# Performance work log

Measured on AMD Instinct MI355X. Metric: run time of the kernel, lower is better.

Reference implementation:

```python
import jax, jax.numpy as jnp
import numpy as np
import math

B, T, C, F = 8, 2048, 1024, 4096
N_LAYER, LAYER_ID = 12, 1


def _init_params(key):
    ks = jax.random.split(key, 16)
    s = 0.02
    ratio_0_to_1 = LAYER_ID / (N_LAYER - 1)
    ratio_1_to_almost0 = 1.0 - LAYER_ID / N_LAYER
    h = np.arange(C, dtype=np.float32)
    decay = -5.0 + 8.0 * (h / (C - 1)) ** (0.7 + 1.3 * ratio_0_to_1)
    zigzag = np.array([((i + 1) % 3 - 1) for i in range(C)], dtype=np.float32) * 0.5
    first = np.ones(C, dtype=np.float32) * math.log(0.3) + zigzag
    xi = (np.arange(C, dtype=np.float32) / C)
    p = {
        'ln1_w': jnp.ones(C), 'ln1_b': jnp.zeros(C),
        'ln2_w': jnp.ones(C), 'ln2_b': jnp.zeros(C),
        'att_time_decay': jnp.asarray(decay),
        'att_time_first': jnp.asarray(first),
        'att_mix_k': jnp.asarray(xi ** ratio_1_to_almost0),
        'att_mix_v': jnp.asarray(xi ** ratio_1_to_almost0 + 0.3 * ratio_0_to_1),
        'att_mix_r': jnp.asarray(xi ** (0.5 * ratio_1_to_almost0)),
        'att_Wk': jax.random.normal(ks[0], (C, C)) * s,
        'att_Wv': jax.random.normal(ks[1], (C, C)) * s,
        'att_Wr': jax.random.normal(ks[2], (C, C)) * s,
        'att_Wo': jax.random.normal(ks[3], (C, C)) * s,
        'ffn_mix_k': jnp.asarray(xi ** ratio_1_to_almost0),
        'ffn_mix_r': jnp.asarray(xi ** ratio_1_to_almost0),
        'ffn_Wk': jax.random.normal(ks[4], (F, C)) * s,
        'ffn_Wr': jax.random.normal(ks[5], (C, C)) * s,
        'ffn_Wv': jax.random.normal(ks[6], (C, F)) * s,
        'short_W': jax.random.normal(ks[7], (C, C)) * s,
    }
    return p


def setup_inputs() -> dict:
    key = jax.random.key(0)
    k1, k2 = jax.random.split(key)
    inp = {'x': jax.random.normal(k1, (B, T, C), dtype=jnp.float32)}
    inp.update(_init_params(k2))
    return inp


def _layernorm(x, w, b, eps=1e-5):
    mu = jnp.mean(x, axis=-1, keepdims=True)
    var = jnp.var(x, axis=-1, keepdims=True)
    return (x - mu) * jax.lax.rsqrt(var + eps) * w + b


def _time_shift(x):
    # ZeroPad2d((0,0,1,-1)): prepend zero row along T, drop last
    return jnp.pad(x, ((0, 0), (1, 0), (0, 0)))[:, :-1]


def _wkv(time_decay, time_first, k, v):
    # numerically-stable WKV recurrence, matching the CUDA kernel math
    w = -jnp.exp(time_decay)  # [C]
    u = time_first            # [C]
    kt = jnp.swapaxes(k, 0, 1)  # [T,B,C]
    vt = jnp.swapaxes(v, 0, 1)
    a0 = jnp.zeros(k.shape[::2] if False else (k.shape[0], k.shape[2]), k.dtype)
    b0 = jnp.zeros_like(a0)
    p0 = jnp.full_like(a0, -1e30)

    def step(carry, kv):
        a, b, p = carry
        k_t, v_t = kv
        ww = u + k_t
        q = jnp.maximum(p, ww)
        e1 = jnp.exp(p - q)
        e2 = jnp.exp(ww - q)
        y = (e1 * a + e2 * v_t) / (e1 * b + e2)
        ww2 = p + w
        q2 = jnp.maximum(ww2, k_t)
        f1 = jnp.exp(ww2 - q2)
        f2 = jnp.exp(k_t - q2)
        return (f1 * a + f2 * v_t, f1 * b + f2, q2), y

    _, ys = jax.lax.scan(step, (a0, b0, p0), (kt, vt))
    return jnp.swapaxes(ys, 0, 1)  # [B,T,C]


def _lin(x, W):
    return jnp.einsum('btc,oc->bto', x, W)


def reference(x, ln1_w, ln1_b, ln2_w, ln2_b,
              att_time_decay, att_time_first, att_mix_k, att_mix_v, att_mix_r,
              att_Wk, att_Wv, att_Wr, att_Wo,
              ffn_mix_k, ffn_mix_r, ffn_Wk, ffn_Wr, ffn_Wv, short_W):
    # --- TimeMix on ln1(x) ---
    h = _layernorm(x, ln1_w, ln1_b)
    hh = _time_shift(h)
    xk = h * att_mix_k + hh * (1 - att_mix_k)
    xv = h * att_mix_v + hh * (1 - att_mix_v)
    xr = h * att_mix_r + hh * (1 - att_mix_r)
    k = _lin(xk, att_Wk)
    v = _lin(xv, att_Wv)
    sr = jax.nn.sigmoid(_lin(xr, att_Wr))
    rwkv = sr * _wkv(att_time_decay, att_time_first, k, v)
    att_out = _lin(rwkv, att_Wo)
    # shortcut linear replaces identity residual (L3TC Block)
    x = _lin(x, short_W) + att_out
    # --- ChannelMix on ln2(x) ---
    g = _layernorm(x, ln2_w, ln2_b)
    gg = _time_shift(g)
    gk = g * ffn_mix_k + gg * (1 - ffn_mix_k)
    gr = g * ffn_mix_r + gg * (1 - ffn_mix_r)
    kk = jnp.square(jax.nn.relu(_lin(gk, ffn_Wk)))
    kv = _lin(kk, ffn_Wv)
    rkv = jax.nn.sigmoid(_lin(gr, ffn_Wr)) * kv
    return x + rkv
```

## Files before the change

### kernel.cpp

```cpp
#include <hip/hip_runtime.h>

#define BB 8
#define TT 2048
#define CC 1024
#define FF 4096
#define MM (BB*TT)

typedef unsigned short u16;
typedef __bf16 bf16x8 __attribute__((ext_vector_type(8)));
typedef float f32x4 __attribute__((ext_vector_type(4)));

__device__ __forceinline__ u16 f2bf(float f) {
  unsigned int u = __float_as_uint(f);
  u += 0x7fffu + ((u >> 16) & 1u);
  return (u16)(u >> 16);
}
__device__ __forceinline__ float bf2f(u16 h) {
  unsigned int u = ((unsigned int)h) << 16;
  return __uint_as_float(u);
}
__device__ __forceinline__ float sigm(float x) { return 1.f / (1.f + __expf(-x)); }

__device__ __forceinline__ void async16(const void* g, void* l) {
  __builtin_amdgcn_global_load_lds(
      (const __attribute__((address_space(1))) unsigned int*)g,
      (__attribute__((address_space(3))) unsigned int*)l, 16, 0, 0);
}

#define GROUP_M 16

#define DSRD(d, a, o) \
  asm volatile("ds_read_b128 %0, %1 offset:%c2" : "=v"(d) : "v"(a), "i"(o))

#define MFMA16(A_, B_, C_) \
  (C_) = __builtin_amdgcn_mfma_f32_16x16x32_bf16( \
      __builtin_bit_cast(bf16x8, (A_)), __builtin_bit_cast(bf16x8, (B_)), (C_), 0, 0, 0)

#define SCHED0  __builtin_amdgcn_sched_barrier(0)
#define BARRIER __builtin_amdgcn_s_barrier()
#define LGKM(n) asm volatile("s_waitcnt lgkmcnt(" #n ")")

#define READ_A4(bank, BETA, MH, KH) do { \
  DSRD(bank[0], aAddr##KH, (BETA)*32768 + ((MH)*4+0)*2048); \
  DSRD(bank[1], aAddr##KH, (BETA)*32768 + ((MH)*4+1)*2048); \
  DSRD(bank[2], aAddr##KH, (BETA)*32768 + ((MH)*4+2)*2048); \
  DSRD(bank[3], aAddr##KH, (BETA)*32768 + ((MH)*4+3)*2048); \
} while (0)

#define READ_B2(bank, BETA, NP, KH) do { \
  DSRD(bank[0], bAddr##KH, (BETA)*32768 + (NP)*16384 + 0*2048); \
  DSRD(bank[1], bAddr##KH, (BETA)*32768 + (NP)*16384 + 1*2048); \
} while (0)

#define MFMA8(ABANK, BBANK, AO, NO) do { \
  _Pragma("unroll") \
  for (int mi = 0; mi < 4; ++mi) \
    _Pragma("unroll") \
    for (int ni = 0; ni < 2; ++ni) \
      MFMA16(ABANK[mi], BBANK[ni], acc[(AO)+mi][(NO)+ni]); \
} while (0)

#define EXEC8(ABANK, BBANK, AO, NO) do { \
  __builtin_amdgcn_s_setprio(1); \
  MFMA8(ABANK, BBANK, AO, NO); \
  __builtin_amdgcn_s_setprio(0); SCHED0; } while (0)

#define TILE(BETA, T2A, ST, RD) do { \
   READ_A4(aB, BETA, 1, 0); \
  LGKM(6); SCHED0; EXEC8(aA, bP, 0, 0); \
   READ_B2(bR, BETA, 0, 1); \
  LGKM(6); SCHED0; EXEC8(aA, bQ, 0, 2); \
   READ_A4(aA, BETA, 0, 1); \
  LGKM(6); SCHED0; EXEC8(aB, bQ, 4, 2); \
  BARRIER; SCHED0; \
   \
  READ_B2(bS, BETA, 1, 1); \
  if (ST) { stB(BETA, 0, T2A); stB(BETA, 1, T2A); \
            stA(BETA, 0, T2A); stA(BETA, 2, T2A); } \
  LGKM(6); SCHED0; EXEC8(aB, bP, 4, 0); \
   READ_A4(aB, BETA, 1, 1); \
  LGKM(6); SCHED0; EXEC8(aA, bR, 0, 0); \
  if (ST) asm volatile("s_waitcnt vmcnt(4)"); \
  else    asm volatile("s_waitcnt vmcnt(0)"); \
  BARRIER; SCHED0; \
   \
  if (RD) READ_B2(bP, (BETA)^1, 0, 0); \
  if (ST) { stB(BETA, 2, T2A); stB(BETA, 3, T2A); \
            stA(BETA, 1, T2A); stA(BETA, 3, T2A); } \
  if (RD) LGKM(6); else LGKM(4); \
  SCHED0; EXEC8(aA, bS, 0, 2); \
   if (RD) { READ_A4(aA, (BETA)^1, 0, 0); LGKM(6); } else LGKM(0); \
  SCHED0; EXEC8(aB, bS, 4, 2); \
   if (RD) { READ_B2(bQ, (BETA)^1, 1, 0); LGKM(8); } else LGKM(0); \
  SCHED0; EXEC8(aB, bR, 4, 0); \
} while (0)

template<int MODE>
__global__ __launch_bounds__(512, 2) void gemm_bt(
    const u16* __restrict__ A, const u16* __restrict__ W,
    float* __restrict__ Cf, u16* __restrict__ Cb,
    const u16* __restrict__ R, int N, int K)
{
  __shared__ __align__(16) u16 ldsA[2][256 * 64];
  __shared__ __align__(16) u16 ldsB[2][256 * 64];

  const int tid  = threadIdx.x;
  const int wave = tid >> 6;
  const int lane = tid & 63;
  const int wmi  = wave >> 2;
  const int wni  = wave & 3;
  const int lm   = lane & 15;
  const int lq   = lane >> 4;

  const int bid  = blockIdx.x + blockIdx.y * gridDim.x;
  const int gsz  = GROUP_M * gridDim.y;
  const int gid  = bid / gsz;
  const int rem  = bid - gid * gsz;
  const int bm   = (gid * GROUP_M + (rem % GROUP_M)) * 256;
  const int bn   = (rem / GROUP_M) * 256;

  const int NT = K >> 6;

  const int ls     = lane >> 3;
  const int schunk = (lane & 7) ^ ls;
  const int rowA   = wave * 8 + ls;
  const int rowB   = (wave >> 2) * 64 + (wave & 3) * 8 + ls;
  const u16* gA = A + (size_t)(bm + rowA) * K + schunk * 8;
  const u16* gB = W + (size_t)(bn + rowB) * K + schunk * 8;
  const size_t rowK = (size_t)64 * K;

  auto stA = [&](int buf, int q, int t2) {
    async16(gA + (size_t)t2 * 64 + (size_t)q * rowK,
            &ldsA[buf][(q * 64 + wave * 8) * 64]);
  };
  auto stB = [&](int buf, int q, int t2) {
    const int qrow = (q == 0) ? 0 : (q == 1) ? 128 : (q == 2) ? 32 : 160;
    async16(gB + (size_t)t2 * 64 + (size_t)qrow * K,
            &ldsB[buf][(q * 64 + wave * 8) * 64]);
  };

  const unsigned lAbase =
      (unsigned)(size_t)(const __attribute__((address_space(3))) u16*)&ldsA[0][0];
  const unsigned lBbase =
      (unsigned)(size_t)(const __attribute__((address_space(3))) u16*)&ldsB[0][0];
  const unsigned aAddr0 = lAbase + (unsigned)((wmi * 128 + lm) * 128 + (((lq    ) ^ (lm & 7)) * 16));
  const unsigned aAddr1 = lAbase + (unsigned)((wmi * 128 + lm) * 128 + (((lq + 4) ^ (lm & 7)) * 16));
  const unsigned bAddr0 = lBbase + (unsigned)((wni * 32 + lm) * 128 + (((lq    ) ^ (lm & 7)) * 16));
  const unsigned bAddr1 = lBbase + (unsigned)((wni * 32 + lm) * 128 + (((lq + 4) ^ (lm & 7)) * 16));

  f32x4 acc[8][4] = {};
  f32x4 aA[4], aB[4], bP[2], bQ[2], bR[2], bS[2];

  stA(0, 0, 0); stA(0, 1, 0); stA(0, 2, 0); stA(0, 3, 0);
  stB(0, 0, 0); stB(0, 1, 0); stB(0, 2, 0); stB(0, 3, 0);
  stA(1, 0, 1); stA(1, 1, 1); stA(1, 2, 1); stA(1, 3, 1);
  stB(1, 0, 1); stB(1, 1, 1); stB(1, 2, 1); stB(1, 3, 1);
  asm volatile("s_waitcnt vmcnt(0)");
  BARRIER;
  READ_A4(aA, 0, 0, 0);
  READ_B2(bP, 0, 0, 0);
  READ_B2(bQ, 0, 1, 0);
  LGKM(0); SCHED0;

  for (int t = 0; t + 3 < NT; t += 2) {
    TILE(0, t + 2, 1, 1);
    TILE(1, t + 3, 1, 1);
  }

  TILE(0, 0, 0, 1);
  TILE(1, 0, 0, 0);

  const int row0 = bm + wmi * 128 + lq * 4;
  const int col0 = bn + wni * 64 + lm;
#pragma unroll
  for (int mi = 0; mi < 8; ++mi)
#pragma unroll
    for (int ni = 0; ni < 4; ++ni) {
      size_t base = (size_t)(row0 + mi * 16) * N + (col0 + ni * 16);
#pragma unroll
      for (int r2 = 0; r2 < 4; ++r2) {
        size_t idx = base + (size_t)r2 * N;
        float v = acc[mi][ni][r2];
        if (MODE == 0) Cf[idx] = v;
        if (MODE == 2) { float rl = v > 0.f ? v : 0.f; Cb[idx] = f2bf(rl * rl); }
        if (MODE == 3) Cb[idx] = f2bf(v);
        if (MODE == 4) Cf[idx] += sigm(bf2f(R[idx])) * v;
      }
    }
}

__global__ __launch_bounds__(256) void prep_mix(
    const float* __restrict__ x,
    const float* __restrict__ lnw, const float* __restrict__ lnb,
    const float* __restrict__ mk, const float* __restrict__ mv, const float* __restrict__ mr,
    u16* __restrict__ ok, u16* __restrict__ ov, u16* __restrict__ orr,
    u16* __restrict__ oxb)
{
  const int m = blockIdx.x;
  const int t = m & (TT - 1);
  const int tid = threadIdx.x;
  const int wave = tid >> 6, lane = tid & 63;
  const bool hasp = (t != 0);

  const float4 xc4 = ((const float4*)(x + (size_t)m * CC))[tid];
  float4 xp4 = make_float4(0.f, 0.f, 0.f, 0.f);
  if (hasp) xp4 = ((const float4*)(x + (size_t)(m - 1) * CC))[tid];

  float s0 = xc4.x + xc4.y + xc4.z + xc4.w;
  float s1 = xc4.x*xc4.x + xc4.y*xc4.y + xc4.z*xc4.z + xc4.w*xc4.w;
  float s2 = xp4.x + xp4.y + xp4.z + xp4.w;
  float s3 = xp4.x*xp4.x + xp4.y*xp4.y + xp4.z*xp4.z + xp4.w*xp4.w;
#pragma unroll
  for (int off2 = 32; off2 > 0; off2 >>= 1) {
    s0 += __shfl_xor(s0, off2);
    s1 += __shfl_xor(s1, off2);
    s2 += __shfl_xor(s2, off2);
    s3 += __shfl_xor(s3, off2);
  }
  __shared__ float red[4][4];
  if (lane == 0) { red[0][wave] = s0; red[1][wave] = s1; red[2][wave] = s2; red[3][wave] = s3; }
  __syncthreads();
  const float S0 = red[0][0] + red[0][1] + red[0][2] + red[0][3];
  const float S1 = red[1][0] + red[1][1] + red[1][2] + red[1][3];
  const float S2 = red[2][0] + red[2][1] + red[2][2] + red[2][3];
  const float S3 = red[3][0] + red[3][1] + red[3][2] + red[3][3];
  const float inv = 1.f / (float)CC;
  const float muc = S0 * inv, varc = S1 * inv - muc * muc, rsc = rsqrtf(varc + 1e-5f);
  const float mup = S2 * inv, varp = S3 * inv - mup * mup, rsp = rsqrtf(varp + 1e-5f);

  const float xc[4] = {xc4.x, xc4.y, xc4.z, xc4.w};
  const float xp[4] = {xp4.x, xp4.y, xp4.z, xp4.w};
  const float4 lw4 = ((const float4*)lnw)[tid];
  const float4 lb4 = ((const float4*)lnb)[tid];
  const float lw[4] = {lw4.x, lw4.y, lw4.z, lw4.w};
  const float lb[4] = {lb4.x, lb4.y, lb4.z, lb4.w};
  const float4 mk4 = ((const float4*)mk)[tid];
  const float mka[4] = {mk4.x, mk4.y, mk4.z, mk4.w};
  const float4 mr4 = ((const float4*)mr)[tid];
  const float mra[4] = {mr4.x, mr4.y, mr4.z, mr4.w};
  float mva[4] = {0.f, 0.f, 0.f, 0.f};
  if (ov) {
    const float4 mv4 = ((const float4*)mv)[tid];
    mva[0] = mv4.x; mva[1] = mv4.y; mva[2] = mv4.z; mva[3] = mv4.w;
  }

  ushort4 wk2, wv2, wr2, wb2;
  u16* pk = (u16*)&wk2; u16* pv = (u16*)&wv2; u16* pr = (u16*)&wr2; u16* pb = (u16*)&wb2;
#pragma unroll
  for (int j = 0; j < 4; ++j) {
    float h  = (xc[j] - muc) * rsc * lw[j] + lb[j];
    float hh = hasp ? (xp[j] - mup) * rsp * lw[j] + lb[j] : 0.f;
    pk[j] = f2bf(h * mka[j] + hh * (1.f - mka[j]));
    pv[j] = f2bf(h * mva[j] + hh * (1.f - mva[j]));
    pr[j] = f2bf(h * mra[j] + hh * (1.f - mra[j]));
    pb[j] = f2bf(xc[j]);
  }
  ((ushort4*)(ok + (size_t)m * CC))[tid] = wk2;
  if (ov)  ((ushort4*)(ov  + (size_t)m * CC))[tid] = wv2;
  ((ushort4*)(orr + (size_t)m * CC))[tid] = wr2;
  if (oxb) ((ushort4*)(oxb + (size_t)m * (2 * CC)))[tid] = wb2;
}

#define WKV_CPB 32
#define WKV_NCH 32
#define WKV_L   (TT / WKV_NCH)

__global__ __launch_bounds__(1024) void wkv_scan(
    const u16* __restrict__ k, const u16* __restrict__ v, const u16* __restrict__ r,
    const float* __restrict__ decay, const float* __restrict__ first,
    u16* __restrict__ out)
{
  const int b  = blockIdx.x >> 5;
  const int c0 = (blockIdx.x & 31) * WKV_CPB;
  const int tid = threadIdx.x;
  const int cl = tid & 31;
  const int j  = tid >> 5;
  const int c  = c0 + cl;

  const float w   = -__expf(decay[c]);
  const float lam = __expf(w);
  const float eu  = __expf(first[c]);

  const size_t base  = (size_t)b * TT * CC + (size_t)j * WKV_L * CC + c;
  size_t obase = ((size_t)b * TT + (size_t)j * WKV_L) * (2 * CC) + c;

  float a = 0.f, bb = 0.f;
  size_t idx = base;
  for (int i = 0; i < WKV_L; ++i, idx += CC) {
    const float kt = bf2f(k[idx]), vt = bf2f(v[idx]);
    const float ek = __expf(kt);
    a  = fmaf(lam, a, ek * vt);
    bb = fmaf(lam, bb, ek);
  }

  __shared__ float sA[WKV_NCH][WKV_CPB];
  __shared__ float sB[WKV_NCH][WKV_CPB];
  sA[j][cl] = a; sB[j][cl] = bb;
  __syncthreads();
  if (tid < WKV_CPB) {
    float ca = 0.f, cb = 0.f;
    const float cw   = -__expf(decay[c0 + tid]);
    const float cLam = __expf(cw * (float)WKV_L);
#pragma unroll
    for (int q = 0; q < WKV_NCH; ++q) {
      const float ta = sA[q][tid], tb = sB[q][tid];
      sA[q][tid] = ca; sB[q][tid] = cb;
      ca = fmaf(cLam, ca, ta);
      cb = fmaf(cLam, cb, tb);
    }
  }
  __syncthreads();
  a = sA[j][cl]; bb = sB[j][cl];

  idx = base;
  for (int i = 0; i < WKV_L; ++i, idx += CC, obase += 2 * CC) {
    const float kt = bf2f(k[idx]), vt = bf2f(v[idx]), rt = bf2f(r[idx]);
    const float ek = __expf(kt);
    const float e2 = eu * ek;
    const float y  = (a + e2 * vt) / (bb + e2);
    out[obase] = f2bf(sigm(rt) * y);
    a  = fmaf(lam, a, ek * vt);
    bb = fmaf(lam, bb, ek);
  }
}

struct ConvArgs { const float* src[8]; int end[8]; int dstoff[8]; };

__global__ __launch_bounds__(256) void conv_w(ConvArgs args, u16* __restrict__ dst)
{
  const int i = (blockIdx.x * 256 + threadIdx.x) * 4;
  int seg = 0;
  const float* sp = args.src[0];
  int base = 0;
#pragma unroll
  for (int s = 1; s < 8; ++s) {
    if (i >= args.end[s - 1]) { seg = s; sp = args.src[s]; base = args.end[s - 1]; }
  }
  const int l = i - base;
  const float4 vv = *(const float4*)(sp + l);
  int dsti;
  if (seg == 3)      { int row = l >> 10, col = l & 1023; dsti = args.dstoff[3] + row * 2048 + 1024 + col; }
  else if (seg == 4) { int row = l >> 10, col = l & 1023; dsti = args.dstoff[4] + row * 2048 + col; }
  else               dsti = args.dstoff[seg] + l;
  ushort4 d;
  d.x = f2bf(vv.x); d.y = f2bf(vv.y); d.z = f2bf(vv.z); d.w = f2bf(vv.w);
  *(ushort4*)(dst + dsti) = d;
}

extern "C" void kernel_launch(void* const* d_in, const int* in_sizes, int n_in,
                              void* d_out, int out_size, void* d_ws, size_t ws_size,
                              hipStream_t stream)
{
  const float* x    = (const float*)d_in[0];
  const float* ln1w = (const float*)d_in[1];
  const float* ln1b = (const float*)d_in[2];
  const float* ln2w = (const float*)d_in[3];
  const float* ln2b = (const float*)d_in[4];
  const float* tdec = (const float*)d_in[5];
  const float* tfir = (const float*)d_in[6];
  const float* amk  = (const float*)d_in[7];
  const float* amv  = (const float*)d_in[8];
  const float* amr  = (const float*)d_in[9];
  const float* Wk   = (const float*)d_in[10];
  const float* Wv   = (const float*)d_in[11];
  const float* Wr   = (const float*)d_in[12];
  const float* Wo   = (const float*)d_in[13];
  const float* fmk  = (const float*)d_in[14];
  const float* fmr  = (const float*)d_in[15];
  const float* WfK  = (const float*)d_in[16];
  const float* WfR  = (const float*)d_in[17];
  const float* WfV  = (const float*)d_in[18];
  const float* Wsh  = (const float*)d_in[19];
  float* out = (float*)d_out;
  char* ws = (char*)d_ws;

  u16* wW = (u16*)(ws);
  u16* U0 = (u16*)(ws + 29360128);
  u16* U1 = (u16*)(ws + 62914560);
  u16* U2 = (u16*)(ws + 96468992);
  u16* U3 = (u16*)(ws + 130023424);
  u16* U4 = (u16*)(ws + 163577856);

  u16* xk   = U0;
  u16* xv   = U1;
  u16* xr   = U2;
  u16* Ap   = U4;
  u16* kbuf = U3;
  u16* vbuf = U0;
  u16* rbuf = U1;
  u16* gk   = U0;
  u16* gr   = U1;
  u16* kkb  = U2;
  u16* rffn = U0;

  u16* bWk   = wW + 0;
  u16* bWv   = wW + 1048576;
  u16* bWr   = wW + 2097152;
  u16* bWsWo = wW + 3145728;
  u16* bWfR  = wW + 5242880;
  u16* bWfK  = wW + 6291456;
  u16* bWfV  = wW + 10485760;

  ConvArgs ca;
  ca.src[0] = Wk;  ca.src[1] = Wv;  ca.src[2] = Wr;  ca.src[3] = Wo;
  ca.src[4] = Wsh; ca.src[5] = WfR; ca.src[6] = WfK; ca.src[7] = WfV;
  const int e = 1048576;
  ca.end[0] = e;     ca.end[1] = 2*e;  ca.end[2] = 3*e;  ca.end[3] = 4*e;
  ca.end[4] = 5*e;   ca.end[5] = 6*e;  ca.end[6] = 10*e; ca.end[7] = 14*e;
  ca.dstoff[0] = 0;     ca.dstoff[1] = e;    ca.dstoff[2] = 2*e;
  ca.dstoff[3] = 3*e;   ca.dstoff[4] = 3*e;
  ca.dstoff[5] = 5*e;   ca.dstoff[6] = 6*e;  ca.dstoff[7] = 10*e;

  conv_w<<<14336, 256, 0, stream>>>(ca, wW);
  prep_mix<<<MM, 256, 0, stream>>>(x, ln1w, ln1b, amk, amv, amr, xk, xv, xr, Ap);

  dim3 g8(MM / 256, CC / 256);
  gemm_bt<3><<<g8, 512, 0, stream>>>(xk, bWk, nullptr, kbuf, nullptr, CC, CC);
  gemm_bt<3><<<g8, 512, 0, stream>>>(xv, bWv, nullptr, vbuf, nullptr, CC, CC);
  gemm_bt<3><<<g8, 512, 0, stream>>>(xr, bWr, nullptr, rbuf, nullptr, CC, CC);

  wkv_scan<<<BB * (CC / WKV_CPB), 1024, 0, stream>>>(kbuf, vbuf, rbuf, tdec, tfir, Ap + CC);

  gemm_bt<0><<<g8, 512, 0, stream>>>(Ap, bWsWo, out, nullptr, nullptr, CC, 2 * CC);

  prep_mix<<<MM, 256, 0, stream>>>(out, ln2w, ln2b, fmk, nullptr, fmr, gk, nullptr, gr, nullptr);

  dim3 gF(MM / 256, FF / 256);
  gemm_bt<2><<<gF, 512, 0, stream>>>(gk, bWfK, nullptr, kkb, nullptr, FF, CC);
  gemm_bt<3><<<g8, 512, 0, stream>>>(gr, bWfR, nullptr, rffn, nullptr, CC, CC);
  gemm_bt<4><<<g8, 512, 0, stream>>>(kkb, bWfV, out, nullptr, rffn, CC, FF);
}
```

Before: 796.4 us.

## Restructure GEMM main loop into four 16-MFMA phases with full-K register banks

Rewrites the double-buffered GEMM tile schedule so each phase loads both K-halves of A/B fragments into registers and issues 16 MFMAs per phase instead of 8. Fine-grained lgkmcnt waits are replaced with full lgkmcnt(0) waits, and all global-to-LDS async stores are moved to the end of the tile after a full vmcnt(0) wait. This aims to reduce scheduling complexity and barrier count per MFMA, but it loses the overlap between LDS reads and MFMAs. It also reduces how far global loads run ahead, and it raises register pressure for the fragment banks.

```diff
diff --git a/kernel.cpp b/kernel.cpp
--- a/kernel.cpp
+++ b/kernel.cpp
@@ -38,61 +38,60 @@
 
 #define SCHED0  __builtin_amdgcn_sched_barrier(0)
 #define BARRIER __builtin_amdgcn_s_barrier()
-#define LGKM(n) asm volatile("s_waitcnt lgkmcnt(" #n ")")
-
-#define READ_A4(bank, BETA, MH, KH) do { \
-  DSRD(bank[0], aAddr##KH, (BETA)*32768 + ((MH)*4+0)*2048); \
-  DSRD(bank[1], aAddr##KH, (BETA)*32768 + ((MH)*4+1)*2048); \
-  DSRD(bank[2], aAddr##KH, (BETA)*32768 + ((MH)*4+2)*2048); \
-  DSRD(bank[3], aAddr##KH, (BETA)*32768 + ((MH)*4+3)*2048); \
+#define LGKM0   asm volatile("s_waitcnt lgkmcnt(0)")
+
+#define READ_A8(bank, BETA, MH) do { \
+  DSRD(bank[0][0], aAddr0, (BETA)*32768 + ((MH)*4+0)*2048); \
+  DSRD(bank[0][1], aAddr1, (BETA)*32768 + ((MH)*4+0)*2048); \
+  DSRD(bank[1][0], aAddr0, (BETA)*32768 + ((MH)*4+1)*2048); \
+  DSRD(bank[1][1], aAddr1, (BETA)*32768 + ((MH)*4+1)*2048); \
+  DSRD(bank[2][0], aAddr0, (BETA)*32768 + ((MH)*4+2)*2048); \
+  DSRD(bank[2][1], aAddr1, (BETA)*32768 + ((MH)*4+2)*2048); \
+  DSRD(bank[3][0], aAddr0, (BETA)*32768 + ((MH)*4+3)*2048); \
+  DSRD(bank[3][1], aAddr1, (BETA)*32768 + ((MH)*4+3)*2048); \
 } while (0)
 
-#define READ_B2(bank, BETA, NP, KH) do { \
-  DSRD(bank[0], bAddr##KH, (BETA)*32768 + (NP)*16384 + 0*2048); \
-  DSRD(bank[1], bAddr##KH, (BETA)*32768 + (NP)*16384 + 1*2048); \
+#define READ_B4(bank, BETA, NP) do { \
+  DSRD(bank[0][0], bAddr0, (BETA)*32768 + (NP)*16384 + 0*2048); \
+  DSRD(bank[0][1], bAddr1, (BETA)*32768 + (NP)*16384 + 0*2048); \
+  DSRD(bank[1][0], bAddr0, (BETA)*32768 + (NP)*16384 + 1*2048); \
+  DSRD(bank[1][1], bAddr1, (BETA)*32768 + (NP)*16384 + 1*2048); \
 } while (0)
 
-#define MFMA8(ABANK, BBANK, AO, NO) do { \
+#define EXEC16(ABANK, BBANK, AO, NO) do { \
+  __builtin_amdgcn_s_setprio(1); \
   _Pragma("unroll") \
   for (int mi = 0; mi < 4; ++mi) \
     _Pragma("unroll") \
     for (int ni = 0; ni < 2; ++ni) \
-      MFMA16(ABANK[mi], BBANK[ni], acc[(AO)+mi][(NO)+ni]); \
-} while (0)
-
-#define EXEC8(ABANK, BBANK, AO, NO) do { \
-  __builtin_amdgcn_s_setprio(1); \
-  MFMA8(ABANK, BBANK, AO, NO); \
+      MFMA16(ABANK[mi][0], BBANK[ni][0], acc[(AO)+mi][(NO)+ni]); \
+  _Pragma("unroll") \
+  for (int mi = 0; mi < 4; ++mi) \
+    _Pragma("unroll") \
+    for (int ni = 0; ni < 2; ++ni) \
+      MFMA16(ABANK[mi][1], BBANK[ni][1], acc[(AO)+mi][(NO)+ni]); \
   __builtin_amdgcn_s_setprio(0); SCHED0; } while (0)
 
 #define TILE(BETA, T2A, ST, RD) do { \
-   READ_A4(aB, BETA, 1, 0); \
-  LGKM(6); SCHED0; EXEC8(aA, bP, 0, 0); \
-   READ_B2(bR, BETA, 0, 1); \
-  LGKM(6); SCHED0; EXEC8(aA, bQ, 0, 2); \
-   READ_A4(aA, BETA, 0, 1); \
-  LGKM(6); SCHED0; EXEC8(aB, bQ, 4, 2); \
+   \
+  LGKM0; SCHED0; EXEC16(a0, b01, 0, 0); \
+  READ_A8(a1, BETA, 1); \
+   \
+  LGKM0; SCHED0; EXEC16(a1, b01, 4, 0); \
+  READ_B4(b23, BETA, 1); \
+  asm volatile("s_waitcnt vmcnt(0)"); \
   BARRIER; SCHED0; \
    \
-  READ_B2(bS, BETA, 1, 1); \
-  if (ST) { stB(BETA, 0, T2A); stB(BETA, 1, T2A); \
-            stA(BETA, 0, T2A); stA(BETA, 2, T2A); } \
-  LGKM(6); SCHED0; EXEC8(aB, bP, 4, 0); \
-   READ_A4(aB, BETA, 1, 1); \
-  LGKM(6); SCHED0; EXEC8(aA, bR, 0, 0); \
-  if (ST) asm volatile("s_waitcnt vmcnt(4)"); \
-  else    asm volatile("s_waitcnt vmcnt(0)"); \
+  LGKM0; SCHED0; EXEC16(a0, b23, 0, 2); \
+  if (RD) READ_B4(b01, (BETA)^1, 0); \
   BARRIER; SCHED0; \
    \
-  if (RD) READ_B2(bP, (BETA)^1, 0, 0); \
-  if (ST) { stB(BETA, 2, T2A); stB(BETA, 3, T2A); \
-            stA(BETA, 1, T2A); stA(BETA, 3, T2A); } \
-  if (RD) LGKM(6); else LGKM(4); \
-  SCHED0; EXEC8(aA, bS, 0, 2); \
-   if (RD) { READ_A4(aA, (BETA)^1, 0, 0); LGKM(6); } else LGKM(0); \
-  SCHED0; EXEC8(aB, bS, 4, 2); \
-   if (RD) { READ_B2(bQ, (BETA)^1, 1, 0); LGKM(8); } else LGKM(0); \
-  SCHED0; EXEC8(aB, bR, 4, 0); \
+  LGKM0; SCHED0; EXEC16(a1, b23, 4, 2); \
+  if (RD) READ_A8(a0, (BETA)^1, 0); \
+  if (ST) { stA(BETA, 0, T2A); stA(BETA, 1, T2A); \
+            stA(BETA, 2, T2A); stA(BETA, 3, T2A); \
+            stB(BETA, 0, T2A); stB(BETA, 1, T2A); \
+            stB(BETA, 2, T2A); stB(BETA, 3, T2A); } \
 } while (0)
 
 template<int MODE>
@@ -149,7 +148,7 @@
   const unsigned bAddr1 = lBbase + (unsigned)((wni * 32 + lm) * 128 + (((lq + 4) ^ (lm & 7)) * 16));
 
   f32x4 acc[8][4] = {};
-  f32x4 aA[4], aB[4], bP[2], bQ[2], bR[2], bS[2];
+  f32x4 a0[4][2], a1[4][2], b01[2][2], b23[2][2];
 
   stA(0, 0, 0); stA(0, 1, 0); stA(0, 2, 0); stA(0, 3, 0);
   stB(0, 0, 0); stB(0, 1, 0); stB(0, 2, 0); stB(0, 3, 0);
@@ -157,10 +156,9 @@
   stB(1, 0, 1); stB(1, 1, 1); stB(1, 2, 1); stB(1, 3, 1);
   asm volatile("s_waitcnt vmcnt(0)");
   BARRIER;
-  READ_A4(aA, 0, 0, 0);
-  READ_B2(bP, 0, 0, 0);
-  READ_B2(bQ, 0, 1, 0);
-  LGKM(0); SCHED0;
+  READ_B4(b01, 0, 0);
+  READ_A8(a0, 0, 0);
+  SCHED0;
 
   for (int t = 0; t + 3 < NT; t += 2) {
     TILE(0, t + 2, 1, 1);
```

Measured after the change: 1.187 ms. 1.49x slower.
